# Kernel optimization log

Measured on AMD Instinct MI355X. Metric: run time of the kernel, lower is better.

Reference implementation:

```python
import jax, jax.numpy as jnp
import numpy as np

ALL_WINDOW_SIZES = [1, 2, 4, 8, 16, 32]
ATTENTION_WINDOW = 32
T, D, N = 8192, 128, 4096
NW = len(ALL_WINDOW_SIZES)


def _layernorm(x, g, b, eps=1e-5):
    mu = x.mean(axis=-1, keepdims=True)
    var = ((x - mu) ** 2).mean(axis=-1, keepdims=True)
    return (x - mu) / jnp.sqrt(var + eps) * g + b


def setup_inputs() -> dict:
    key = jax.random.key(0)
    ks = jax.random.split(key, 16)
    s = 0.02
    return {
        "inputEmbeds": jax.random.normal(ks[0], (T, D), dtype=jnp.float32),
        # per-neuron weights stacked -> Linear(D, N)
        "neuronW": jax.random.normal(ks[1], (D, N), dtype=jnp.float32) * s,
        "neuronB": jnp.zeros((N,), dtype=jnp.float32),
        # tiny attention layer (single head, Q/K/V projections)
        "Wq": jax.random.normal(ks[2], (D, D), dtype=jnp.float32) * s,
        "bq": jnp.zeros((D,), dtype=jnp.float32),
        "Wk": jax.random.normal(ks[3], (D, D), dtype=jnp.float32) * s,
        "bk": jnp.zeros((D,), dtype=jnp.float32),
        "Wv": jax.random.normal(ks[4], (D, D), dtype=jnp.float32) * s,
        "bv": jnp.zeros((D,), dtype=jnp.float32),
        # attentionProjection = LayerNorm(D) -> Linear(D, N)
        "ln_g": jnp.ones((D,), dtype=jnp.float32),
        "ln_b": jnp.zeros((D,), dtype=jnp.float32),
        "projW": jax.random.normal(ks[5], (D, N), dtype=jnp.float32) * s,
        "projb": jnp.zeros((N,), dtype=jnp.float32),
        "windowWeighting": jnp.ones((NW,), dtype=jnp.float32),
        # combinationLayer: Linear(N*NW, N)
        "comboW": jax.random.normal(ks[6], (N * NW, N), dtype=jnp.float32) * 0.005,
        "combob": jnp.zeros((N,), dtype=jnp.float32),
    }


def _tiny_attn(x, Wq, bq, Wk, bk, Wv, bv):
    # x: [B, W, D] -> single-head self attention
    q = x @ Wq + bq
    k = x @ Wk + bk
    v = x @ Wv + bv
    scores = jnp.einsum("bqd,bkd->bqk", q, k) / jnp.sqrt(jnp.asarray(x.shape[-1], x.dtype))
    return jnp.einsum("bqk,bkd->bqd", jax.nn.softmax(scores, axis=-1), v)


def reference(inputEmbeds, neuronW, neuronB, Wq, bq, Wk, bk, Wv, bv,
              ln_g, ln_b, projW, projb, windowWeighting, comboW, combob):
    # all neurons over all tokens: [T, N], tanh activation, clamp to [-5, 5]
    acts = jnp.clip(jnp.tanh(inputEmbeds @ neuronW + neuronB), -5.0, 5.0)

    window_means = []
    for w in ALL_WINDOW_SIZES:
        if w == ATTENTION_WINDOW:
            xw = inputEmbeds[-w:][None]  # [1, w, D]
            attended = _tiny_attn(xw, Wq, bq, Wk, bk, Wv, bv)  # [1, w, D]
            attn_mean = attended.mean(axis=1)  # [1, D]
            proj = _layernorm(attn_mean, ln_g, ln_b) @ projW + projb  # [1, N]
            window_means.append(proj)
        else:
            window_means.append(acts[-w:].mean(axis=0, keepdims=True))  # [1, N]

    norm_w = (windowWeighting + 0.1) / (windowWeighting.sum() + 0.1)
    weighted = jnp.concatenate(
        [window_means[i] * norm_w[i] for i in range(NW)], axis=1)  # [1, N*NW]
    return weighted @ comboW + combob  # [1, N]
```

## Files before the change

kernel.cpp:

```cpp
#include <hip/hip_runtime.h>

#define T_TOK 8192
#define D_DIM 128
#define N_NEU 4096
#define RPC 48
#define NCHUNK 512

typedef float f4_t __attribute__((ext_vector_type(4)));

struct SmemActs {
    float xs16[16][128];
    float wst[32][256];
};
struct SmemQkv {
    float xs[32][128];
    float w[128][128];
};
union SmemA {
    SmemActs a;
    SmemQkv q;
};

__global__ void acts_qkv_kernel(
    const float* __restrict__ x,
    const float* __restrict__ neuronW, const float* __restrict__ neuronB,
    const float* __restrict__ Wq, const float* __restrict__ bq,
    const float* __restrict__ Wk, const float* __restrict__ bk,
    const float* __restrict__ Wv, const float* __restrict__ bv,
    const float* __restrict__ ww,
    float* __restrict__ v,
    float* __restrict__ qkv)
{
    __shared__ SmemA sm;
    const int tid = threadIdx.x;
    const int bid = blockIdx.x;

    if (bid < 16) {
        const int n0 = bid * 256;
        const int n = n0 + tid;
        for (int idx = tid; idx < 16 * 128; idx += 256) {
            int t = idx >> 7, d = idx & 127;
            sm.a.xs16[t][d] = x[(size_t)(T_TOK - 16 + t) * D_DIM + d];
        }
        float acc[16];
        float bias = neuronB[n];
#pragma unroll
        for (int t = 0; t < 16; ++t) acc[t] = bias;
        const f4_t* W4 = reinterpret_cast<const f4_t*>(neuronW);
        f4_t* wst4 = reinterpret_cast<f4_t*>(&sm.a.wst[0][0]);
        for (int c = 0; c < 4; ++c) {
            const int d0 = c * 32;
            __syncthreads();
#pragma unroll
            for (int k = 0; k < 8; ++k) {
                int idx = tid + k * 256;
                int dd = idx >> 6, j4 = idx & 63;
                wst4[dd * 64 + j4] = W4[(size_t)(d0 + dd) * 1024 + (n0 >> 2) + j4];
            }
            __syncthreads();
#pragma unroll
            for (int dd = 0; dd < 32; ++dd) {
                float w = sm.a.wst[dd][tid];
#pragma unroll
                for (int t = 0; t < 16; ++t) acc[t] += sm.a.xs16[t][d0 + dd] * w;
            }
        }
#pragma unroll
        for (int t = 0; t < 16; ++t) acc[t] = tanhf(acc[t]);
        float denom = 0.1f;
#pragma unroll
        for (int i = 0; i < 6; ++i) denom += ww[i];
        const float inv = 1.f / denom;
        float s1 = acc[15];
        float s2 = s1 + acc[14];
        float s4 = s2 + acc[13] + acc[12];
        float s8 = s4 + acc[11] + acc[10] + acc[9] + acc[8];
        float s16 = s8 + acc[7] + acc[6] + acc[5] + acc[4] + acc[3] + acc[2] + acc[1] + acc[0];
        v[0 * N_NEU + n] = s1 * ((ww[0] + 0.1f) * inv);
        v[1 * N_NEU + n] = s2 * 0.5f * ((ww[1] + 0.1f) * inv);
        v[2 * N_NEU + n] = s4 * 0.25f * ((ww[2] + 0.1f) * inv);
        v[3 * N_NEU + n] = s8 * 0.125f * ((ww[3] + 0.1f) * inv);
        v[4 * N_NEU + n] = s16 * 0.0625f * ((ww[4] + 0.1f) * inv);
        return;
    }

    const int m = bid - 16;
    const float* Wm = (m == 0) ? Wq : ((m == 1) ? Wk : Wv);
    const float* bb = (m == 0) ? bq : ((m == 1) ? bk : bv);

    f4_t* xs4 = reinterpret_cast<f4_t*>(&sm.q.xs[0][0]);
    const f4_t* X4 = reinterpret_cast<const f4_t*>(x + (size_t)(T_TOK - 32) * D_DIM);
#pragma unroll
    for (int k = 0; k < 4; ++k) xs4[tid + k * 256] = X4[tid + k * 256];
    f4_t* w4 = reinterpret_cast<f4_t*>(&sm.q.w[0][0]);
    const f4_t* Wm4 = reinterpret_cast<const f4_t*>(Wm);
#pragma unroll
    for (int k = 0; k < 16; ++k) w4[tid + k * 256] = Wm4[tid + k * 256];
    __syncthreads();

    const int d = tid & 127;
    const int g = tid >> 7;
    float acc[16];
    float bias = bb[d];
#pragma unroll
    for (int i = 0; i < 16; ++i) acc[i] = bias;
#pragma unroll 4
    for (int e = 0; e < 128; ++e) {
        float w = sm.q.w[e][d];
#pragma unroll
        for (int i = 0; i < 16; ++i) acc[i] += sm.q.xs[g * 16 + i][e] * w;
    }
#pragma unroll
    for (int i = 0; i < 16; ++i) qkv[m * 4096 + (g * 16 + i) * 128 + d] = acc[i];
}

struct SmemAP {
    union {
        struct {
            float qs[32][128];
            float kt[128][33];
            float vs[32][128];
            float ps[32][33];
            float pbar[32];
            float mvec[128];
            float red[2];
        } a;
        struct {
            float wst[32][256];
        } p;
    } u;
    float ys[128];
};

__global__ void attn_proj_kernel(
    const float* __restrict__ qkv,
    const float* __restrict__ ln_g, const float* __restrict__ ln_b,
    const float* __restrict__ projW,
    const float* __restrict__ projb,
    const float* __restrict__ ww,
    float* __restrict__ v)
{
    __shared__ SmemAP sm;
    const int tid = threadIdx.x;

    for (int idx = tid; idx < 32 * 128; idx += 256) {
        int i = idx >> 7, d = idx & 127;
        sm.u.a.qs[i][d] = qkv[idx];
        sm.u.a.kt[d][i] = qkv[4096 + idx];
        sm.u.a.vs[i][d] = qkv[8192 + idx];
    }
    __syncthreads();
    const float scale = 0.08838834764831845f;
#pragma unroll
    for (int rep = 0; rep < 4; ++rep) {
        int idx = tid + rep * 256;
        int i = idx >> 5, j = idx & 31;
        float acc = 0.f;
        for (int e = 0; e < 128; ++e) acc += sm.u.a.qs[i][e] * sm.u.a.kt[e][j];
        sm.u.a.ps[i][j] = acc * scale;
    }
    __syncthreads();
    if (tid < 32) {
        float mx = -1e30f;
        for (int j = 0; j < 32; ++j) mx = fmaxf(mx, sm.u.a.ps[tid][j]);
        float s = 0.f;
        for (int j = 0; j < 32; ++j) { float e = expf(sm.u.a.ps[tid][j] - mx); sm.u.a.ps[tid][j] = e; s += e; }
        float inv = 1.f / s;
        for (int j = 0; j < 32; ++j) sm.u.a.ps[tid][j] *= inv;
    }
    __syncthreads();
    if (tid < 32) {
        float s = 0.f;
        for (int i = 0; i < 32; ++i) s += sm.u.a.ps[i][tid];
        sm.u.a.pbar[tid] = s * (1.f / 32.f);
    }
    __syncthreads();
    if (tid < 128) {
        float s = 0.f;
        for (int j = 0; j < 32; ++j) s += sm.u.a.pbar[j] * sm.u.a.vs[j][tid];
        sm.u.a.mvec[tid] = s;
    }
    __syncthreads();
    if (tid < 64) {
        float p = sm.u.a.mvec[tid] + sm.u.a.mvec[tid + 64];
        for (int off = 32; off; off >>= 1) p += __shfl_down(p, off);
        if (tid == 0) sm.u.a.red[0] = p * (1.f / 128.f);
    }
    __syncthreads();
    float mu = sm.u.a.red[0];
    if (tid < 64) {
        float t1 = sm.u.a.mvec[tid] - mu, t2 = sm.u.a.mvec[tid + 64] - mu;
        float p = t1 * t1 + t2 * t2;
        for (int off = 32; off; off >>= 1) p += __shfl_down(p, off);
        if (tid == 0) sm.u.a.red[1] = rsqrtf(p * (1.f / 128.f) + 1e-5f);
    }
    __syncthreads();
    if (tid < 128) {
        sm.ys[tid] = (sm.u.a.mvec[tid] - mu) * sm.u.a.red[1] * ln_g[tid] + ln_b[tid];
    }
    __syncthreads();

    const int n0 = blockIdx.x * 256;
    const int n = n0 + tid;
    float denom = 0.1f;
#pragma unroll
    for (int i = 0; i < 6; ++i) denom += ww[i];
    const float nw5 = (ww[5] + 0.1f) / denom;

    float acc = projb[n];
    const f4_t* P4 = reinterpret_cast<const f4_t*>(projW);
    f4_t* wst4 = reinterpret_cast<f4_t*>(&sm.u.p.wst[0][0]);
    for (int c = 0; c < 4; ++c) {
        const int d0 = c * 32;
        __syncthreads();
#pragma unroll
        for (int k = 0; k < 8; ++k) {
            int idx = tid + k * 256;
            int dd = idx >> 6, j4 = idx & 63;
            wst4[dd * 64 + j4] = P4[(size_t)(d0 + dd) * 1024 + (n0 >> 2) + j4];
        }
        __syncthreads();
#pragma unroll
        for (int dd = 0; dd < 32; ++dd) {
            acc += sm.ys[d0 + dd] * sm.u.p.wst[dd][tid];
        }
    }
    v[5 * N_NEU + n] = acc * nw5;
}

__global__ __launch_bounds__(256) void combo_partial_kernel(
    const float* __restrict__ v,
    const float* __restrict__ comboW,
    float* __restrict__ part)
{
    __shared__ float vsm[RPC];
    const int tid = threadIdx.x;
    const int chunk = blockIdx.x >> 2;
    const int cb = blockIdx.x & 3;
    const int row0 = chunk * RPC;

    if (tid < RPC) vsm[tid] = v[row0 + tid];
    __syncthreads();

    const f4_t* W4 = reinterpret_cast<const f4_t*>(comboW);
    const size_t base = (size_t)row0 * 1024 + cb * 256 + tid;
    f4_t acc = {0.f, 0.f, 0.f, 0.f};
#pragma unroll 8
    for (int r = 0; r < RPC; ++r) {
        f4_t w = __builtin_nontemporal_load(&W4[base + (size_t)r * 1024]);
        acc += w * vsm[r];
    }
    reinterpret_cast<f4_t*>(part)[(size_t)chunk * 1024 + cb * 256 + tid] = acc;
}

__global__ void combo_reduce_kernel(const float* __restrict__ part,
                                    const float* __restrict__ bias,
                                    float* __restrict__ out)
{
    __shared__ f4_t red[8][32];
    const int tid = threadIdx.x;
    const int h = tid >> 5;
    const int j = tid & 31;
    const int n4 = blockIdx.x * 32 + j;
    const f4_t* P4 = reinterpret_cast<const f4_t*>(part);
    f4_t acc = {0.f,0.f,0.f,0.f};
#pragma unroll 8
    for (int c = h * 64; c < h * 64 + 64; ++c)
        acc += P4[(size_t)c * 1024 + n4];
    red[h][j] = acc;
    __syncthreads();
    if (h == 0) {
        f4_t s = red[0][j] + red[1][j] + red[2][j] + red[3][j]
               + red[4][j] + red[5][j] + red[6][j] + red[7][j];
        s += reinterpret_cast<const f4_t*>(bias)[n4];
        reinterpret_cast<f4_t*>(out)[n4] = s;
    }
}

extern "C" void kernel_launch(void* const* d_in, const int* in_sizes, int n_in,
                              void* d_out, int out_size, void* d_ws, size_t ws_size,
                              hipStream_t stream) {
    const float* inputEmbeds = (const float*)d_in[0];
    const float* neuronW     = (const float*)d_in[1];
    const float* neuronB     = (const float*)d_in[2];
    const float* Wq          = (const float*)d_in[3];
    const float* bq          = (const float*)d_in[4];
    const float* Wk          = (const float*)d_in[5];
    const float* bk          = (const float*)d_in[6];
    const float* Wv          = (const float*)d_in[7];
    const float* bv          = (const float*)d_in[8];
    const float* ln_g        = (const float*)d_in[9];
    const float* ln_b        = (const float*)d_in[10];
    const float* projW       = (const float*)d_in[11];
    const float* projb       = (const float*)d_in[12];
    const float* ww          = (const float*)d_in[13];
    const float* comboW      = (const float*)d_in[14];
    const float* combob      = (const float*)d_in[15];
    float* out = (float*)d_out;
    float* ws  = (float*)d_ws;

    float* v    = ws;
    float* qkv  = ws + 24576;
    float* part = ws + 36864;

    acts_qkv_kernel<<<19, 256, 0, stream>>>(inputEmbeds, neuronW, neuronB,
                                            Wq, bq, Wk, bk, Wv, bv, ww, v, qkv);
    attn_proj_kernel<<<16, 256, 0, stream>>>(qkv, ln_g, ln_b, projW, projb, ww, v);
    combo_partial_kernel<<<NCHUNK * 4, 256, 0, stream>>>(v, comboW, part);
    combo_reduce_kernel<<<32, 256, 0, stream>>>(part, combob, out);
}
```

Baseline: 112.8 us.

## Fuse attention projection into combo partial kernel and enlarge row chunks

Removes the separate attention/projection kernel launch. The blocks whose rows belong to the sixth (attention) segment now recompute the tiny attention, layernorm and a 128-column slice of the projection inside the combo GEMV kernel. Rows per chunk grow from 48 to 128, giving fewer partials for the reduce kernel. The first chunks switch from nontemporal to ordinary loads, presumably to keep that part of comboW cached. The trade-off is redundant attention work in 128 blocks (4 column-blocks per chunk repeat it) and a longer critical path for those blocks.

```diff
diff --git a/kernel.cpp b/kernel.cpp
--- a/kernel.cpp
+++ b/kernel.cpp
@@ -3,8 +3,10 @@
 #define T_TOK 8192
 #define D_DIM 128
 #define N_NEU 4096
-#define RPC 48
-#define NCHUNK 512
+#define RPC 128
+#define NCHUNK 192
+#define SEG5_CHUNK0 160
+#define PLAIN_LIMIT 96
 
 typedef float f4_t __attribute__((ext_vector_type(4)));
 
@@ -114,141 +116,141 @@
     for (int i = 0; i < 16; ++i) qkv[m * 4096 + (g * 16 + i) * 128 + d] = acc[i];
 }
 
-struct SmemAP {
+struct SmemC {
     union {
         struct {
             float qs[32][128];
             float kt[128][33];
-            float vs[32][128];
             float ps[32][33];
             float pbar[32];
             float mvec[128];
             float red[2];
         } a;
         struct {
-            float wst[32][256];
+            float wst[32][128];
         } p;
     } u;
     float ys[128];
+    float vsm[RPC];
 };
 
-__global__ void attn_proj_kernel(
+__global__ __launch_bounds__(256) void combo_partial_kernel(
+    const float* __restrict__ v,
     const float* __restrict__ qkv,
     const float* __restrict__ ln_g, const float* __restrict__ ln_b,
     const float* __restrict__ projW,
     const float* __restrict__ projb,
     const float* __restrict__ ww,
-    float* __restrict__ v)
-{
-    __shared__ SmemAP sm;
-    const int tid = threadIdx.x;
-
-    for (int idx = tid; idx < 32 * 128; idx += 256) {
-        int i = idx >> 7, d = idx & 127;
-        sm.u.a.qs[i][d] = qkv[idx];
-        sm.u.a.kt[d][i] = qkv[4096 + idx];
-        sm.u.a.vs[i][d] = qkv[8192 + idx];
-    }
-    __syncthreads();
-    const float scale = 0.08838834764831845f;
-#pragma unroll
-    for (int rep = 0; rep < 4; ++rep) {
-        int idx = tid + rep * 256;
-        int i = idx >> 5, j = idx & 31;
-        float acc = 0.f;
-        for (int e = 0; e < 128; ++e) acc += sm.u.a.qs[i][e] * sm.u.a.kt[e][j];
-        sm.u.a.ps[i][j] = acc * scale;
-    }
-    __syncthreads();
-    if (tid < 32) {
-        float mx = -1e30f;
-        for (int j = 0; j < 32; ++j) mx = fmaxf(mx, sm.u.a.ps[tid][j]);
-        float s = 0.f;
-        for (int j = 0; j < 32; ++j) { float e = expf(sm.u.a.ps[tid][j] - mx); sm.u.a.ps[tid][j] = e; s += e; }
-        float inv = 1.f / s;
-        for (int j = 0; j < 32; ++j) sm.u.a.ps[tid][j] *= inv;
-    }
-    __syncthreads();
-    if (tid < 32) {
-        float s = 0.f;
-        for (int i = 0; i < 32; ++i) s += sm.u.a.ps[i][tid];
-        sm.u.a.pbar[tid] = s * (1.f / 32.f);
-    }
-    __syncthreads();
-    if (tid < 128) {
-        float s = 0.f;
-        for (int j = 0; j < 32; ++j) s += sm.u.a.pbar[j] * sm.u.a.vs[j][tid];
-        sm.u.a.mvec[tid] = s;
-    }
-    __syncthreads();
-    if (tid < 64) {
-        float p = sm.u.a.mvec[tid] + sm.u.a.mvec[tid + 64];
-        for (int off = 32; off; off >>= 1) p += __shfl_down(p, off);
-        if (tid == 0) sm.u.a.red[0] = p * (1.f / 128.f);
-    }
-    __syncthreads();
-    float mu = sm.u.a.red[0];
-    if (tid < 64) {
-        float t1 = sm.u.a.mvec[tid] - mu, t2 = sm.u.a.mvec[tid + 64] - mu;
-        float p = t1 * t1 + t2 * t2;
-        for (int off = 32; off; off >>= 1) p += __shfl_down(p, off);
-        if (tid == 0) sm.u.a.red[1] = rsqrtf(p * (1.f / 128.f) + 1e-5f);
-    }
-    __syncthreads();
-    if (tid < 128) {
-        sm.ys[tid] = (sm.u.a.mvec[tid] - mu) * sm.u.a.red[1] * ln_g[tid] + ln_b[tid];
-    }
-    __syncthreads();
-
-    const int n0 = blockIdx.x * 256;
-    const int n = n0 + tid;
-    float denom = 0.1f;
-#pragma unroll
-    for (int i = 0; i < 6; ++i) denom += ww[i];
-    const float nw5 = (ww[5] + 0.1f) / denom;
-
-    float acc = projb[n];
-    const f4_t* P4 = reinterpret_cast<const f4_t*>(projW);
-    f4_t* wst4 = reinterpret_cast<f4_t*>(&sm.u.p.wst[0][0]);
-    for (int c = 0; c < 4; ++c) {
-        const int d0 = c * 32;
-        __syncthreads();
-#pragma unroll
-        for (int k = 0; k < 8; ++k) {
-            int idx = tid + k * 256;
-            int dd = idx >> 6, j4 = idx & 63;
-            wst4[dd * 64 + j4] = P4[(size_t)(d0 + dd) * 1024 + (n0 >> 2) + j4];
-        }
-        __syncthreads();
-#pragma unroll
-        for (int dd = 0; dd < 32; ++dd) {
-            acc += sm.ys[d0 + dd] * sm.u.p.wst[dd][tid];
-        }
-    }
-    v[5 * N_NEU + n] = acc * nw5;
-}
-
-__global__ __launch_bounds__(256) void combo_partial_kernel(
-    const float* __restrict__ v,
     const float* __restrict__ comboW,
     float* __restrict__ part)
 {
-    __shared__ float vsm[RPC];
+    __shared__ SmemC sm;
     const int tid = threadIdx.x;
     const int chunk = blockIdx.x >> 2;
     const int cb = blockIdx.x & 3;
     const int row0 = chunk * RPC;
 
-    if (tid < RPC) vsm[tid] = v[row0 + tid];
+    if (chunk < SEG5_CHUNK0) {
+        if (tid < RPC) sm.vsm[tid] = v[row0 + tid];
+    } else {
+        for (int idx = tid; idx < 32 * 128; idx += 256) {
+            int i = idx >> 7, d = idx & 127;
+            sm.u.a.qs[i][d] = qkv[idx];
+            sm.u.a.kt[d][i] = qkv[4096 + idx];
+        }
+        __syncthreads();
+        const float scale = 0.08838834764831845f;
+#pragma unroll
+        for (int rep = 0; rep < 4; ++rep) {
+            int idx = tid + rep * 256;
+            int i = idx >> 5, j = idx & 31;
+            float acc = 0.f;
+            for (int e = 0; e < 128; ++e) acc += sm.u.a.qs[i][e] * sm.u.a.kt[e][j];
+            sm.u.a.ps[i][j] = acc * scale;
+        }
+        __syncthreads();
+        if (tid < 32) {
+            float mx = -1e30f;
+            for (int j = 0; j < 32; ++j) mx = fmaxf(mx, sm.u.a.ps[tid][j]);
+            float s = 0.f;
+            for (int j = 0; j < 32; ++j) { float e = expf(sm.u.a.ps[tid][j] - mx); sm.u.a.ps[tid][j] = e; s += e; }
+            float inv = 1.f / s;
+            for (int j = 0; j < 32; ++j) sm.u.a.ps[tid][j] *= inv;
+        }
+        __syncthreads();
+        if (tid < 32) {
+            float s = 0.f;
+            for (int i = 0; i < 32; ++i) s += sm.u.a.ps[i][tid];
+            sm.u.a.pbar[tid] = s * (1.f / 32.f);
+        }
+        __syncthreads();
+        if (tid < 128) {
+            float s = 0.f;
+            for (int j = 0; j < 32; ++j) s += sm.u.a.pbar[j] * qkv[8192 + j * 128 + tid];
+            sm.u.a.mvec[tid] = s;
+        }
+        __syncthreads();
+        if (tid < 64) {
+            float p = sm.u.a.mvec[tid] + sm.u.a.mvec[tid + 64];
+            for (int off = 32; off; off >>= 1) p += __shfl_down(p, off);
+            if (tid == 0) sm.u.a.red[0] = p * (1.f / 128.f);
+        }
+        __syncthreads();
+        float mu = sm.u.a.red[0];
+        if (tid < 64) {
+            float t1 = sm.u.a.mvec[tid] - mu, t2 = sm.u.a.mvec[tid + 64] - mu;
+            float p = t1 * t1 + t2 * t2;
+            for (int off = 32; off; off >>= 1) p += __shfl_down(p, off);
+            if (tid == 0) sm.u.a.red[1] = rsqrtf(p * (1.f / 128.f) + 1e-5f);
+        }
+        __syncthreads();
+        if (tid < 128) {
+            sm.ys[tid] = (sm.u.a.mvec[tid] - mu) * sm.u.a.red[1] * ln_g[tid] + ln_b[tid];
+        }
+        __syncthreads();
+
+        const int m0 = row0 & 4095;
+        float denom = 0.1f;
+#pragma unroll
+        for (int i = 0; i < 6; ++i) denom += ww[i];
+        const float nw5 = (ww[5] + 0.1f) / denom;
+
+        float acc = (tid < 128) ? projb[m0 + tid] : 0.f;
+        const f4_t* P4 = reinterpret_cast<const f4_t*>(projW);
+        f4_t* wst4 = reinterpret_cast<f4_t*>(&sm.u.p.wst[0][0]);
+        for (int c = 0; c < 4; ++c) {
+            const int d0 = c * 32;
+            __syncthreads();
+#pragma unroll
+            for (int k = 0; k < 4; ++k) {
+                int idx = tid + k * 256;
+                int dd = idx >> 5, j4 = idx & 31;
+                wst4[dd * 32 + j4] = P4[(size_t)(d0 + dd) * 1024 + (m0 >> 2) + j4];
+            }
+            __syncthreads();
+            if (tid < 128) {
+#pragma unroll
+                for (int dd = 0; dd < 32; ++dd)
+                    acc += sm.ys[d0 + dd] * sm.u.p.wst[dd][tid];
+            }
+        }
+        if (tid < 128) sm.vsm[tid] = acc * nw5;
+    }
     __syncthreads();
 
     const f4_t* W4 = reinterpret_cast<const f4_t*>(comboW);
     const size_t base = (size_t)row0 * 1024 + cb * 256 + tid;
     f4_t acc = {0.f, 0.f, 0.f, 0.f};
+    if (chunk < PLAIN_LIMIT) {
 #pragma unroll 8
-    for (int r = 0; r < RPC; ++r) {
-        f4_t w = __builtin_nontemporal_load(&W4[base + (size_t)r * 1024]);
-        acc += w * vsm[r];
+        for (int r = 0; r < RPC; ++r)
+            acc += W4[base + (size_t)r * 1024] * sm.vsm[r];
+    } else {
+#pragma unroll 8
+        for (int r = 0; r < RPC; ++r) {
+            f4_t w = __builtin_nontemporal_load(&W4[base + (size_t)r * 1024]);
+            acc += w * sm.vsm[r];
+        }
     }
     reinterpret_cast<f4_t*>(part)[(size_t)chunk * 1024 + cb * 256 + tid] = acc;
 }
@@ -265,7 +267,7 @@
     const f4_t* P4 = reinterpret_cast<const f4_t*>(part);
     f4_t acc = {0.f,0.f,0.f,0.f};
 #pragma unroll 8
-    for (int c = h * 64; c < h * 64 + 64; ++c)
+    for (int c = h * 24; c < h * 24 + 24; ++c)
         acc += P4[(size_t)c * 1024 + n4];
     red[h][j] = acc;
     __syncthreads();
@@ -305,7 +307,8 @@
 
     acts_qkv_kernel<<<19, 256, 0, stream>>>(inputEmbeds, neuronW, neuronB,
                                             Wq, bq, Wk, bk, Wv, bv, ww, v, qkv);
-    attn_proj_kernel<<<16, 256, 0, stream>>>(qkv, ln_g, ln_b, projW, projb, ww, v);
-    combo_partial_kernel<<<NCHUNK * 4, 256, 0, stream>>>(v, comboW, part);
+    combo_partial_kernel<<<NCHUNK * 4, 256, 0, stream>>>(v, qkv, ln_g, ln_b,
+                                                         projW, projb, ww,
+                                                         comboW, part);
     combo_reduce_kernel<<<32, 256, 0, stream>>>(part, combob, out);
 }
```

New measurement: 111.5 us. No clear change (-1.2%).
